# Performance work log

Hardware: AMD Instinct MI355X
Metric: run time of the kernel (lower is better)

Reference implementation:

```python
import jax, jax.numpy as jnp
import numpy as np

B, N, QD = 2, 2048, 1024
HEADS, DIM_HEAD = 16, 64
INNER = HEADS * DIM_HEAD  # 1024
SCALE = DIM_HEAD ** -0.5


def setup_inputs() -> dict:
    key = jax.random.key(0)
    ks = jax.random.split(key, 8)
    x = jax.random.normal(ks[0], (B, N, QD), dtype=jnp.float32)
    bias = jax.random.normal(ks[1], (B, N, N), dtype=jnp.float32)
    mask = jax.random.randint(ks[2], (B, N), 0, 2) > 0
    # parameters (nn.Linear stores weight [out, in]; we keep [in, out] and matmul x @ W)
    Wq = jax.random.normal(ks[3], (QD, INNER), dtype=jnp.float32) * (QD ** -0.5)
    Wkv = jax.random.normal(ks[4], (QD, 2 * INNER), dtype=jnp.float32) * (QD ** -0.5)
    Wo = jax.random.normal(ks[5], (INNER, QD), dtype=jnp.float32) * (INNER ** -0.5)
    bo = jax.random.normal(ks[6], (QD,), dtype=jnp.float32) * 0.01
    return {"x": x, "bias": bias, "mask": mask, "Wq": Wq, "Wkv": Wkv, "Wo": Wo, "bo": bo}


def reference(x, bias, mask, Wq, Wkv, Wo, bo):
    b, n, _ = x.shape
    q = x @ Wq                      # [b, n, inner]
    kv = x @ Wkv                    # [b, n, 2*inner] (context defaults to x)
    k, v = jnp.split(kv, 2, axis=-1)
    # split heads: [b, h, n, d]
    split = lambda t: t.reshape(b, n, HEADS, DIM_HEAD).transpose(0, 2, 1, 3)
    q, k, v = split(q), split(k), split(v)
    sim = jnp.einsum('bhid,bhjd->bhij', q, k) * SCALE   # [b, h, n, n]
    sim = sim + bias[:, None, :, :]                      # additive bias broadcast over heads
    max_neg = -jnp.finfo(sim.dtype).max
    sim = jnp.where(mask[:, None, None, :], sim, max_neg)  # per-key mask
    attn = jax.nn.softmax(sim, axis=-1)
    out = jnp.einsum('bhij,bhjd->bhid', attn, v)         # [b, h, n, d]
    out = out.transpose(0, 2, 1, 3).reshape(b, n, INNER)  # merge heads
    return out @ Wo + bo
```

## Files before the change

### kernel.cpp

```cpp
#include <hip/hip_runtime.h>
#include <hip/hip_bf16.h>
#include <stdint.h>

#define B_     2
#define N_     2048
#define QD_    1024
#define H_     16
#define DH_    64
#define INNER_ 1024
#define SCALE_ 0.125f
#define LOG2E_ 1.44269504f
#define QS_    (SCALE_ * LOG2E_)

typedef unsigned short u16;
typedef __attribute__((ext_vector_type(8))) short bf16x8;
typedef __attribute__((ext_vector_type(4))) float f32x4;
typedef __attribute__((ext_vector_type(4))) unsigned short u16x4;
typedef __attribute__((ext_vector_type(8))) unsigned short u16x8;

#define GLD16(gp, lp) __builtin_amdgcn_global_load_lds( \
    (const __attribute__((address_space(1))) unsigned int*)(gp), \
    (__attribute__((address_space(3))) unsigned int*)(lp), 16, 0, 0)

__device__ inline u16 f2bf(float f) {
    union { float f; uint32_t u; } c; c.f = f;
    uint32_t r = c.u + 0x7FFFu + ((c.u >> 16) & 1u);
    return (u16)(r >> 16);
}
__device__ inline float bf2f(u16 s) {
    union { uint32_t u; float f; } c; c.u = ((uint32_t)s) << 16;
    return c.f;
}
__device__ inline void split2(float v, u16 &h, u16 &l) {
    u16 hs = f2bf(v);
    h = hs;
    l = f2bf(v - bf2f(hs));
}
__device__ inline unsigned pk2(float a, float b) {
    float2 f; f.x = a; f.y = b;
    union { __hip_bfloat162 v; unsigned u; } c;
    c.v = __float22bfloat162_rn(f);
    return c.u;
}
__device__ inline float f4get(const float4& v, int r) {
    return r == 0 ? v.x : r == 1 ? v.y : r == 2 ? v.z : v.w;
}

__global__ __launch_bounds__(256) void prep_kernel(
    const float* __restrict__ x, u16* __restrict__ xh, u16* __restrict__ xl,
    const float* __restrict__ Wq, const float* __restrict__ Wkv, const float* __restrict__ Wo,
    u16* __restrict__ wTh, u16* __restrict__ wTl,
    u16* __restrict__ woTh, u16* __restrict__ woTl)
{
    __shared__ float t[32][33];
    const int blk = blockIdx.x, tid = threadIdx.x;
    if (blk < 4096) {
        int idx = blk * 256 + tid;
        float4 v = ((const float4*)x)[idx];
        u16x4 hv, lv; u16 h, l;
        split2(v.x, h, l); hv.x = h; lv.x = l;
        split2(v.y, h, l); hv.y = h; lv.y = l;
        split2(v.z, h, l); hv.z = h; lv.z = l;
        split2(v.w, h, l); hv.w = h; lv.w = l;
        ((u16x4*)xh)[idx] = hv;
        ((u16x4*)xl)[idx] = lv;
        return;
    }
    int local = blk - 4096;
    const float* src; u16 *dhi, *dlo; int C, bx, by;
    if (local < 1024)      { src = Wq;  dhi = wTh;                dlo = wTl;                C = 1024; by = local >> 5; bx = local & 31; }
    else if (local < 3072) { int l2 = local - 1024; src = Wkv; dhi = wTh + 1024 * 1024; dlo = wTl + 1024 * 1024; C = 2048; by = l2 >> 6; bx = l2 & 63; }
    else                   { int l2 = local - 3072; src = Wo;  dhi = woTh;               dlo = woTl;               C = 1024; by = l2 >> 5; bx = l2 & 31; }
    const int x0 = bx * 32, y0 = by * 32;
    const int tx = tid & 31, ty = tid >> 5;
    for (int yy = ty; yy < 32; yy += 8)
        t[yy][tx] = src[(size_t)(y0 + yy) * C + x0 + tx];
    __syncthreads();
    for (int i = ty; i < 32; i += 8) {
        float v = t[tx][i];
        u16 h, l; split2(v, h, l);
        size_t o = (size_t)(x0 + i) * 1024 + y0 + tx;
        dhi[o] = h; dlo[o] = l;
    }
}

__device__ inline void bias_read(int T, int bkoff, int bl16,
                                 const float* __restrict__ bias,
                                 const int* __restrict__ mask,
                                 float4 bR[4], int4& bM)
{
    int bb2 = T >> 10, rest = T & 1023;
    int k0b = (rest & 31) * 64, q0 = (rest >> 5) * 64;
    int kk = k0b + bkoff;
    bM = *(const int4*)&mask[bb2 * N_ + kk];
#pragma unroll
    for (int m = 0; m < 4; m++)
        bR[m] = *(const float4*)&bias[((size_t)bb2 * N_ + q0 + m * 16 + bl16) * N_ + kk];
}
__device__ inline void bias_store(int T, int bwvr, int blane, int bhf,
                                  const float4 bR[4], const int4& bM,
                                  u16* __restrict__ bsw)
{
    int bb2 = T >> 10, rest = T & 1023;
    int k0b = (rest & 31) * 64, q0 = (rest >> 5) * 64;
    int wv = ((k0b >> 5) & 3) + bwvr;
    const u16 NEG = f2bf(-1e30f);
    const int mok[4] = { bM.x, bM.y, bM.z, bM.w };
    u16x8 o0, o1;
#pragma unroll
    for (int i = 0; i < 8; i++) {
        int m = i >> 2, r = i & 3;
        o0[i] = mok[r] ? f2bf(f4get(bR[m], r) * LOG2E_) : NEG;
    }
#pragma unroll
    for (int i = 0; i < 8; i++) {
        int m = 2 + (i >> 2), r = i & 3;
        o1[i] = mok[r] ? f2bf(f4get(bR[m], r) * LOG2E_) : NEG;
    }
    size_t ob = ((((size_t)bb2 * 32 + (q0 >> 6)) * 16 + (k0b >> 7)) * 4 + wv) * 2048
                + (size_t)blane * 32 + bhf * 16;
    *(u16x8*)&bsw[ob]     = o0;
    *(u16x8*)&bsw[ob + 8] = o1;
}
__device__ inline void bias_block(int T, int tid,
                                  const float* __restrict__ bias,
                                  const int* __restrict__ mask,
                                  u16* __restrict__ bsw)
{
    const int bp = tid >> 1, bhf = tid & 1;
    const int blane = bp & 63, bquad = blane >> 4, bl16 = blane & 15;
    const int bwvr = bp >> 6;
    const int bkoff = bwvr * 32 + bquad * 8 + bhf * 4;
    float4 bR[4]; int4 bM;
    bias_read(T, bkoff, bl16, bias, mask, bR, bM);
    bias_store(T, bwvr, blane, bhf, bR, bM, bsw);
}

__global__ __launch_bounds__(256) void gemm_qkv_bias(
    int mode,
    const u16* __restrict__ Ah, const u16* __restrict__ Al,
    const u16* __restrict__ Bh,
    u16* __restrict__ qh,
    u16* __restrict__ kb, u16* __restrict__ vT,
    const float* __restrict__ bias, const int* __restrict__ mask,
    u16* __restrict__ bsw)
{
    __shared__ __align__(16) char smem[32768];
    const int tid = threadIdx.x;

    int gid = -1, bid = -1;
    if (mode == 1) {
        const int i = blockIdx.x;
        if (i < 1280) {
            int g = i % 5;
            if (g < 4) gid = (i / 5) * 4 + g;
            else       bid = i / 5;
        } else {
            bid = i - 1024;
        }
    } else if (mode == 0) gid = blockIdx.x;
    else bid = blockIdx.x;

    if (bid >= 0) {
        bias_block(bid, tid, bias, mask, bsw);
        return;
    }
    gid = (gid & 7) * 128 + (gid >> 3);

    const int wave = tid >> 6, lane = tid & 63;
    const int quad = lane >> 4, l16 = lane & 15;
    const int wm = wave >> 1, wn = wave & 1;
    const int row0 = tid >> 2, g4 = tid & 3;
    const int gc1 = (g4 ^ (row0 & 3)) * 8, gc2 = (g4 ^ ((row0 + 64) & 3)) * 8;
    const int ldsw = wave * 1024;

    if (gid < 512) {
        const int bm = (gid >> 4) * 128, bn = (8 + (gid & 15)) * 128;
        f32x4 acc[4][4];
#pragma unroll
        for (int i = 0; i < 4; i++)
#pragma unroll
            for (int j = 0; j < 4; j++) acc[i][j] = (f32x4){0.f, 0.f, 0.f, 0.f};

        const size_t a1 = (size_t)(bm + row0) * 1024 + gc1, a2 = (size_t)(bm + row0 + 64) * 1024 + gc2;
        const size_t b1 = (size_t)(bn + row0) * 1024 + gc1, b2 = (size_t)(bn + row0 + 64) * 1024 + gc2;

        auto issue = [&](char* base, int kn) {
            GLD16(Ah + a1 + kn, base + ldsw);
            GLD16(Ah + a2 + kn, base + 4096 + ldsw);
            GLD16(Bh + b1 + kn, base + 8192 + ldsw);
            GLD16(Bh + b2 + kn, base + 12288 + ldsw);
        };

        issue(smem, 0);
        int cur = 0;
        for (int k0 = 0; k0 < 1024; k0 += 32) {
            __syncthreads();
            char* cb_ = smem + cur * 16384;
            if (k0 + 32 < 1024) issue(smem + (cur ^ 1) * 16384, k0 + 32);
            const u16* cA = (const u16*)cb_;
            const u16* cB = (const u16*)(cb_ + 8192);
            bf16x8 fa[4], fb[4];
#pragma unroll
            for (int s = 0; s < 4; s++) {
                int ra = wm * 64 + s * 16 + l16;
                int rb = wn * 64 + s * 16 + l16;
                fa[s] = *(const bf16x8*)&cA[ra * 32 + (quad ^ (ra & 3)) * 8];
                fb[s] = *(const bf16x8*)&cB[rb * 32 + (quad ^ (rb & 3)) * 8];
            }
#pragma unroll
            for (int sm = 0; sm < 4; sm++)
#pragma unroll
                for (int sn = 0; sn < 4; sn++)
                    acc[sm][sn] = __builtin_amdgcn_mfma_f32_16x16x32_bf16(fa[sm], fb[sn], acc[sm][sn], 0, 0, 0);
            cur ^= 1;
        }
#pragma unroll
        for (int sm = 0; sm < 4; sm++) {
            int rowb = bm + wm * 64 + sm * 16 + quad * 4;
            int bb = rowb >> 11, i0 = rowb & 2047;
#pragma unroll
            for (int sn = 0; sn < 4; sn++) {
                int col = bn + wn * 64 + sn * 16 + l16;
                int region = col >> 10;
                int hh = (col >> 6) & 15;
                int d = col & 63;
                if (region == 1) {
#pragma unroll
                    for (int r = 0; r < 4; r++) {
                        size_t o = (((size_t)(bb * H_ + hh)) * N_ + i0 + r) * DH_ + d;
                        kb[o] = f2bf(acc[sm][sn][r]);
                    }
                } else {
                    u16x4 pv;
#pragma unroll
                    for (int r = 0; r < 4; r++) pv[r] = f2bf(acc[sm][sn][r]);
                    *(u16x4*)&vT[(((size_t)(bb * H_ + hh)) * DH_ + d) * N_ + i0] = pv;
                }
            }
        }
    } else {
        const int g2 = gid - 512;
        const int bm = (g2 >> 3) * 64, bn = (g2 & 7) * 128;
        f32x4 acc[2][4];
#pragma unroll
        for (int i = 0; i < 2; i++)
#pragma unroll
            for (int j = 0; j < 4; j++) acc[i][j] = (f32x4){0.f, 0.f, 0.f, 0.f};

        const size_t a1 = (size_t)(bm + row0) * 1024 + gc1;
        const size_t b1 = (size_t)(bn + row0) * 1024 + gc1, b2 = (size_t)(bn + row0 + 64) * 1024 + gc2;

        auto issue = [&](char* base, int kn) {
            GLD16(Ah + a1 + kn, base + ldsw);
            GLD16(Al + a1 + kn, base + 4096 + ldsw);
            GLD16(Bh + b1 + kn, base + 8192 + ldsw);
            GLD16(Bh + b2 + kn, base + 12288 + ldsw);
        };

        issue(smem, 0);
        int cur = 0;
        for (int k0 = 0; k0 < 1024; k0 += 32) {
            __syncthreads();
            char* cb_ = smem + cur * 16384;
            if (k0 + 32 < 1024) issue(smem + (cur ^ 1) * 16384, k0 + 32);
            const u16* cAh = (const u16*)cb_;
            const u16* cAl = (const u16*)(cb_ + 4096);
            const u16* cB  = (const u16*)(cb_ + 8192);
            bf16x8 fah[2], fal[2], fb[4];
#pragma unroll
            for (int s = 0; s < 2; s++) {
                int ra = wm * 32 + s * 16 + l16;
                int ca = (quad ^ (ra & 3)) * 8;
                fah[s] = *(const bf16x8*)&cAh[ra * 32 + ca];
                fal[s] = *(const bf16x8*)&cAl[ra * 32 + ca];
            }
#pragma unroll
            for (int s = 0; s < 4; s++) {
                int rb = wn * 64 + s * 16 + l16;
                fb[s] = *(const bf16x8*)&cB[rb * 32 + (quad ^ (rb & 3)) * 8];
            }
#pragma unroll
            for (int sm = 0; sm < 2; sm++)
#pragma unroll
                for (int sn = 0; sn < 4; sn++) {
                    acc[sm][sn] = __builtin_amdgcn_mfma_f32_16x16x32_bf16(fah[sm], fb[sn], acc[sm][sn], 0, 0, 0);
                    acc[sm][sn] = __builtin_amdgcn_mfma_f32_16x16x32_bf16(fal[sm], fb[sn], acc[sm][sn], 0, 0, 0);
                }
            cur ^= 1;
        }
#pragma unroll
        for (int sm = 0; sm < 2; sm++) {
            int rowb = bm + wm * 32 + sm * 16 + quad * 4;
            int bb = rowb >> 11, i0 = rowb & 2047;
#pragma unroll
            for (int sn = 0; sn < 4; sn++) {
                int col = bn + wn * 64 + sn * 16 + l16;
                int hh = col >> 6, d = col & 63;
#pragma unroll
                for (int r = 0; r < 4; r++) {
                    size_t o = (((size_t)(bb * H_ + hh)) * N_ + i0 + r) * DH_ + d;
                    qh[o] = f2bf(acc[sm][sn][r] * QS_);
                }
            }
        }
    }
}

__global__ __launch_bounds__(256) void gemm_out(
    const u16* __restrict__ Ab,
    const u16* __restrict__ Bh,
    const float* __restrict__ bo, float* __restrict__ out)
{
    __shared__ __align__(16) char smem[24576];
    const int tid = threadIdx.x;
    const int wave = tid >> 6, lane = tid & 63;
    const int quad = lane >> 4, l16 = lane & 15;
    const int wm = wave >> 1, wn = wave & 1;
    const int bm = blockIdx.y * 128, bn = blockIdx.x * 64;

    f32x4 acc[4][2];
#pragma unroll
    for (int i = 0; i < 4; i++)
#pragma unroll
        for (int j = 0; j < 2; j++) acc[i][j] = (f32x4){0.f, 0.f, 0.f, 0.f};

    const int row0 = tid >> 2, g4 = tid & 3;
    const int r1 = row0, r2 = row0 + 64;
    const int gc1 = (g4 ^ (r1 & 3)) * 8, gc2 = (g4 ^ (r2 & 3)) * 8;
    const size_t a1 = (size_t)(bm + r1) * 1024 + gc1, a2 = (size_t)(bm + r2) * 1024 + gc2;
    const size_t bgo = (size_t)(bn + r1) * 1024 + gc1;
    const int ldsw = wave * 1024;

    auto issue = [&](char* base, int kn) {
        GLD16(Ab + a1 + kn, base + ldsw);
        GLD16(Ab + a2 + kn, base + 4096 + ldsw);
        GLD16(Bh + bgo + kn, base + 8192 + ldsw);
    };

    issue(smem, 0);
    int cur = 0;
    for (int k0 = 0; k0 < 1024; k0 += 32) {
        __syncthreads();
        char* cb_ = smem + cur * 12288;
        if (k0 + 32 < 1024) issue(smem + (cur ^ 1) * 12288, k0 + 32);
        const u16* cA  = (const u16*)cb_;
        const u16* cBh = (const u16*)(cb_ + 8192);
        bf16x8 fa[4], fbh[2];
#pragma unroll
        for (int s = 0; s < 4; s++) {
            int ra = wm * 64 + s * 16 + l16;
            int ca = (quad ^ (ra & 3)) * 8;
            fa[s] = *(const bf16x8*)&cA[ra * 32 + ca];
        }
#pragma unroll
        for (int s = 0; s < 2; s++) {
            int rb = wn * 32 + s * 16 + l16;
            int cb = (quad ^ (rb & 3)) * 8;
            fbh[s] = *(const bf16x8*)&cBh[rb * 32 + cb];
        }
#pragma unroll
        for (int sm = 0; sm < 4; sm++)
#pragma unroll
            for (int sn = 0; sn < 2; sn++)
                acc[sm][sn] = __builtin_amdgcn_mfma_f32_16x16x32_bf16(fa[sm], fbh[sn], acc[sm][sn], 0, 0, 0);
        cur ^= 1;
    }
#pragma unroll
    for (int sm = 0; sm < 4; sm++) {
        int rowb = bm + wm * 64 + sm * 16 + quad * 4;
#pragma unroll
        for (int sn = 0; sn < 2; sn++) {
            int col = bn + wn * 32 + sn * 16 + l16;
            float bv = bo[col];
#pragma unroll
            for (int r = 0; r < 4; r++)
                out[(size_t)(rowb + r) * 1024 + col] = acc[sm][sn][r] + bv;
        }
    }
}

#define LDK 72
#define LDV 128

__global__ __launch_bounds__(256, 2) void attn_kernel(
    const u16* __restrict__ qh,
    const u16* __restrict__ kb, const u16* __restrict__ vT,
    const u16* __restrict__ bsw, u16* __restrict__ ob)
{
    __shared__ __align__(16) char smem[35328];
    u16* sK  = (u16*)smem;
    u16* sVt = (u16*)(smem + 18432);
    float* rO = (float*)smem;
    float* rL = (float*)(smem + 34816);

    const int bh = blockIdx.y, b = bh >> 4, h = bh & 15;
    const int qt = blockIdx.x, qbase = qt * 64;
    const int tid = threadIdx.x, wave = tid >> 6, lane = tid & 63;
    const int quad = lane >> 4, l16 = lane & 15;

    bf16x8 aq[4][2];
#pragma unroll
    for (int m = 0; m < 4; m++) {
        size_t qo = ((size_t)bh * N_ + qbase + m * 16 + l16) * DH_ + quad * 8;
        aq[m][0] = *(const bf16x8*)&qh[qo];
        aq[m][1] = *(const bf16x8*)&qh[qo + 32];
    }
    f32x4 Oacc[4][4], lacc[4];
#pragma unroll
    for (int m = 0; m < 4; m++) {
        lacc[m] = (f32x4){0.f, 0.f, 0.f, 0.f};
#pragma unroll
        for (int nd = 0; nd < 4; nd++) Oacc[m][nd] = (f32x4){0.f, 0.f, 0.f, 0.f};
    }
    bf16x8 ones;
#pragma unroll
    for (int i = 0; i < 8; i++) ones[i] = (short)0x3F80;

    const int rK = tid >> 3, cK = (tid & 7) * 8;
    const int sigK = ((rK & 4) << 2) + ((rK >> 3) << 2) + (rK & 3);
    const int rV = tid >> 4;
    const int vg = tid & 15;
    const int cV = vg * 8;
    const int vsw = (vg ^ (rV & 7)) * 8;
    const int vrg = ((wave * 4 + quad) ^ (l16 & 7)) * 8;
    const size_t kgbase = (size_t)bh * N_ * DH_;
    const size_t vgbase = (size_t)bh * DH_ * N_;
    const size_t bswb = (size_t)(b * 32 + qt) * 131072 + (size_t)wave * 2048
                        + (size_t)lane * 32;

    bf16x8 pK[4], pV[4];
    u16x8 cB[4], nB[4];
#pragma unroll
    for (int it = 0; it < 4; it++) {
        pK[it] = *(const bf16x8*)&kb[kgbase + (size_t)(rK + it * 32) * DH_ + cK];
        pV[it] = *(const bf16x8*)&vT[vgbase + (size_t)(rV + it * 16) * N_ + cV];
    }
#pragma unroll
    for (int c = 0; c < 4; c++) cB[c] = *(const u16x8*)&bsw[bswb + c * 8];

    for (int jt = 0; jt < 16; jt++) {
#pragma unroll
        for (int it = 0; it < 4; it++) {
            *(bf16x8*)&sK[(it * 32 + sigK) * LDK + cK] = pK[it];
            *(bf16x8*)&sVt[(rV + it * 16) * LDV + vsw] = pV[it];
        }
        __syncthreads();
        if (jt < 15) {
            int j0n = (jt + 1) * 128;
#pragma unroll
            for (int it = 0; it < 4; it++) {
                pK[it] = *(const bf16x8*)&kb[kgbase + (size_t)(j0n + rK + it * 32) * DH_ + cK];
                pV[it] = *(const bf16x8*)&vT[vgbase + (size_t)(rV + it * 16) * N_ + j0n + cV];
            }
            size_t bb = bswb + (size_t)(jt + 1) * 8192;
#pragma unroll
            for (int c = 0; c < 4; c++) nB[c] = *(const u16x8*)&bsw[bb + c * 8];
        }
        bf16x8 kf[2][2], vf[4];
#pragma unroll
        for (int n = 0; n < 2; n++)
#pragma unroll
            for (int s = 0; s < 2; s++)
                kf[n][s] = *(const bf16x8*)&sK[(wave * 32 + n * 16 + l16) * LDK + s * 32 + quad * 8];
#pragma unroll
        for (int nd = 0; nd < 4; nd++)
            vf[nd] = *(const bf16x8*)&sVt[(nd * 16 + l16) * LDV + vrg];

#pragma unroll
        for (int m = 0; m < 4; m++) {
            f32x4 S0, S1;
#pragma unroll
            for (int r = 0; r < 4; r++) {
                S0[r] = bf2f(cB[m >> 1][(m & 1) * 4 + r]);
                S1[r] = bf2f(cB[2 + (m >> 1)][(m & 1) * 4 + r]);
            }
#pragma unroll
            for (int s = 0; s < 2; s++) {
                S0 = __builtin_amdgcn_mfma_f32_16x16x32_bf16(kf[0][s], aq[m][s], S0, 0, 0, 0);
                S1 = __builtin_amdgcn_mfma_f32_16x16x32_bf16(kf[1][s], aq[m][s], S1, 0, 0, 0);
            }
            float p0[4], p1[4];
#pragma unroll
            for (int r = 0; r < 4; r++) {
                p0[r] = __builtin_amdgcn_exp2f(S0[r]);
                p1[r] = __builtin_amdgcn_exp2f(S1[r]);
            }
            union { bf16x8 v; unsigned w[4]; } pa;
            pa.w[0] = pk2(p0[0], p0[1]);
            pa.w[1] = pk2(p0[2], p0[3]);
            pa.w[2] = pk2(p1[0], p1[1]);
            pa.w[3] = pk2(p1[2], p1[3]);
            lacc[m] = __builtin_amdgcn_mfma_f32_16x16x32_bf16(pa.v, ones, lacc[m], 0, 0, 0);
#pragma unroll
            for (int nd = 0; nd < 4; nd++)
                Oacc[m][nd] = __builtin_amdgcn_mfma_f32_16x16x32_bf16(pa.v, vf[nd], Oacc[m][nd], 0, 0, 0);
        }
#pragma unroll
        for (int c = 0; c < 4; c++) cB[c] = nB[c];
        __syncthreads();
    }

    if (wave >= 2) {
        int slot = wave - 2;
#pragma unroll
        for (int m = 0; m < 4; m++) {
#pragma unroll
            for (int nd = 0; nd < 4; nd++)
#pragma unroll
                for (int r = 0; r < 4; r++)
                    rO[(slot * 64 + m * 16 + quad * 4 + r) * 68 + nd * 16 + l16] = Oacc[m][nd][r];
            if (l16 == 0)
#pragma unroll
                for (int r = 0; r < 4; r++)
                    rL[slot * 64 + m * 16 + quad * 4 + r] = lacc[m][r];
        }
    }
    __syncthreads();
    if (wave < 2) {
        int slot = wave;
#pragma unroll
        for (int m = 0; m < 4; m++) {
#pragma unroll
            for (int nd = 0; nd < 4; nd++)
#pragma unroll
                for (int r = 0; r < 4; r++) {
                    int idx = (slot * 64 + m * 16 + quad * 4 + r) * 68 + nd * 16 + l16;
                    rO[idx] += Oacc[m][nd][r];
                }
            if (l16 == 0)
#pragma unroll
                for (int r = 0; r < 4; r++)
                    rL[slot * 64 + m * 16 + quad * 4 + r] += lacc[m][r];
        }
    }
    __syncthreads();
    {
        const int q = tid >> 2, dg = (tid & 3) * 16;
        float l = rL[q] + rL[64 + q];
        float inv = 1.f / l;
        f32x4 s[4];
#pragma unroll
        for (int i4 = 0; i4 < 4; i4++) {
            s[i4] = *(const f32x4*)&rO[(size_t)q * 68 + dg + i4 * 4];
            f32x4 v = *(const f32x4*)&rO[(size_t)(64 + q) * 68 + dg + i4 * 4];
            s[i4] += v;
        }
        size_t obase = ((size_t)b * N_ + qbase + q) * INNER_ + h * 64 + dg;
#pragma unroll
        for (int i4 = 0; i4 < 4; i4++) {
            u16x4 o4;
#pragma unroll
            for (int r = 0; r < 4; r++) o4[r] = f2bf(s[i4][r] * inv);
            *(u16x4*)&ob[obase + i4 * 4] = o4;
        }
    }
}

extern "C" void kernel_launch(void* const* d_in, const int* in_sizes, int n_in,
                              void* d_out, int out_size, void* d_ws, size_t ws_size,
                              hipStream_t stream)
{
    const float* x    = (const float*)d_in[0];
    const float* bias = (const float*)d_in[1];
    const int*   mask = (const int*)d_in[2];
    const float* Wq   = (const float*)d_in[3];
    const float* Wkv  = (const float*)d_in[4];
    const float* Wo   = (const float*)d_in[5];
    const float* bo   = (const float*)d_in[6];
    float* out = (float*)d_out;

    char* w = (char*)d_ws;
    const size_t MB = 1024 * 1024;
    u16* q_h   = (u16*)(w);
    u16* k_b   = (u16*)(w + 16 * MB);
    u16* v_T   = (u16*)(w + 24 * MB);
    u16* xs_h  = (u16*)(w + 32 * MB);
    u16* xs_l  = (u16*)(w + 40 * MB);
    u16* wT_h  = (u16*)(w + 48 * MB);
    u16* wT_l  = (u16*)(w + 54 * MB);
    u16* woT_h = (u16*)(w + 60 * MB);
    u16* woT_l = (u16*)(w + 62 * MB);
    u16* o_b   = (u16*)(w + 64 * MB);

    const size_t bsw_bytes = (size_t)2 * N_ * N_ * sizeof(u16);
    const bool concurrent = ws_size >= 72 * MB + bsw_bytes;

    prep_kernel<<<8192, 256, 0, stream>>>(x, xs_h, xs_l, Wq, Wkv, Wo, wT_h, wT_l, woT_h, woT_l);

    if (concurrent) {
        u16* bsw = (u16*)(w + 72 * MB);
        gemm_qkv_bias<<<3072, 256, 0, stream>>>(1, xs_h, xs_l, wT_h,
                                                q_h, k_b, v_T, bias, mask, bsw);
        attn_kernel<<<dim3(32, 32), 256, 0, stream>>>(q_h, k_b, v_T, bsw, o_b);
    } else {
        u16* bsw = (u16*)(w + 32 * MB);
        gemm_qkv_bias<<<1024, 256, 0, stream>>>(0, xs_h, xs_l, wT_h,
                                                q_h, k_b, v_T, bias, mask, bsw);
        gemm_qkv_bias<<<2048, 256, 0, stream>>>(2, xs_h, xs_l, wT_h,
                                                q_h, k_b, v_T, bias, mask, bsw);
        attn_kernel<<<dim3(32, 32), 256, 0, stream>>>(q_h, k_b, v_T, bsw, o_b);
    }
    gemm_out<<<dim3(16, 32), 256, 0, stream>>>(o_b, woT_h, bo, out);
}
```

Measured before the change: 233.2 us.

## Split attention work across 8 waves by key group and query half

The attention kernel now launches 512 threads per block. Each wave owns one of four key sub-tiles and one of two query halves, so it holds half the Q fragments and accumulators it held before. The K/V staging loads and the bias reads are redistributed over the extra threads, and the epilogue writes 8-wide bf16 stores. The aim is more waves to hide latency and lower per-thread register pressure, at the cost of each wave re-reading the same K/V LDS fragments and more threads meeting at each barrier.

```diff
diff --git a/kernel.cpp b/kernel.cpp
--- a/kernel.cpp
+++ b/kernel.cpp
@@ -383,7 +383,7 @@
 #define LDK 72
 #define LDV 128
 
-__global__ __launch_bounds__(256, 2) void attn_kernel(
+__global__ __launch_bounds__(512, 2) void attn_kernel(
     const u16* __restrict__ qh,
     const u16* __restrict__ kb, const u16* __restrict__ vT,
     const u16* __restrict__ bsw, u16* __restrict__ ob)
@@ -398,87 +398,88 @@
     const int qt = blockIdx.x, qbase = qt * 64;
     const int tid = threadIdx.x, wave = tid >> 6, lane = tid & 63;
     const int quad = lane >> 4, l16 = lane & 15;
-
-    bf16x8 aq[4][2];
-#pragma unroll
-    for (int m = 0; m < 4; m++) {
-        size_t qo = ((size_t)bh * N_ + qbase + m * 16 + l16) * DH_ + quad * 8;
-        aq[m][0] = *(const bf16x8*)&qh[qo];
-        aq[m][1] = *(const bf16x8*)&qh[qo + 32];
-    }
-    f32x4 Oacc[4][4], lacc[4];
-#pragma unroll
-    for (int m = 0; m < 4; m++) {
-        lacc[m] = (f32x4){0.f, 0.f, 0.f, 0.f};
-#pragma unroll
-        for (int nd = 0; nd < 4; nd++) Oacc[m][nd] = (f32x4){0.f, 0.f, 0.f, 0.f};
+    const int kg = wave & 3, mg = wave >> 2;
+
+    bf16x8 aq[2][2];
+#pragma unroll
+    for (int mm = 0; mm < 2; mm++) {
+        size_t qo = ((size_t)bh * N_ + qbase + (mg * 2 + mm) * 16 + l16) * DH_ + quad * 8;
+        aq[mm][0] = *(const bf16x8*)&qh[qo];
+        aq[mm][1] = *(const bf16x8*)&qh[qo + 32];
+    }
+    f32x4 Oacc[2][4], lacc[2];
+#pragma unroll
+    for (int mm = 0; mm < 2; mm++) {
+        lacc[mm] = (f32x4){0.f, 0.f, 0.f, 0.f};
+#pragma unroll
+        for (int nd = 0; nd < 4; nd++) Oacc[mm][nd] = (f32x4){0.f, 0.f, 0.f, 0.f};
     }
     bf16x8 ones;
 #pragma unroll
     for (int i = 0; i < 8; i++) ones[i] = (short)0x3F80;
 
     const int rK = tid >> 3, cK = (tid & 7) * 8;
-    const int sigK = ((rK & 4) << 2) + ((rK >> 3) << 2) + (rK & 3);
+    const int sigK = (rK & 32) + ((rK & 4) << 2) + (((rK >> 3) & 3) << 2) + (rK & 3);
     const int rV = tid >> 4;
     const int vg = tid & 15;
     const int cV = vg * 8;
     const int vsw = (vg ^ (rV & 7)) * 8;
-    const int vrg = ((wave * 4 + quad) ^ (l16 & 7)) * 8;
+    const int vrg = ((kg * 4 + quad) ^ (l16 & 7)) * 8;
     const size_t kgbase = (size_t)bh * N_ * DH_;
     const size_t vgbase = (size_t)bh * DH_ * N_;
-    const size_t bswb = (size_t)(b * 32 + qt) * 131072 + (size_t)wave * 2048
-                        + (size_t)lane * 32;
-
-    bf16x8 pK[4], pV[4];
-    u16x8 cB[4], nB[4];
-#pragma unroll
-    for (int it = 0; it < 4; it++) {
-        pK[it] = *(const bf16x8*)&kb[kgbase + (size_t)(rK + it * 32) * DH_ + cK];
-        pV[it] = *(const bf16x8*)&vT[vgbase + (size_t)(rV + it * 16) * N_ + cV];
-    }
-#pragma unroll
-    for (int c = 0; c < 4; c++) cB[c] = *(const u16x8*)&bsw[bswb + c * 8];
+    const size_t bswb = (size_t)(b * 32 + qt) * 131072 + (size_t)kg * 2048
+                        + (size_t)lane * 32 + (size_t)mg * 8;
+
+    bf16x8 pK[2], pV[2];
+    u16x8 cB[2], nB[2];
+#pragma unroll
+    for (int it = 0; it < 2; it++) {
+        pK[it] = *(const bf16x8*)&kb[kgbase + (size_t)(rK + it * 64) * DH_ + cK];
+        pV[it] = *(const bf16x8*)&vT[vgbase + (size_t)(rV + it * 32) * N_ + cV];
+    }
+#pragma unroll
+    for (int c = 0; c < 2; c++) cB[c] = *(const u16x8*)&bsw[bswb + c * 16];
 
     for (int jt = 0; jt < 16; jt++) {
 #pragma unroll
-        for (int it = 0; it < 4; it++) {
-            *(bf16x8*)&sK[(it * 32 + sigK) * LDK + cK] = pK[it];
-            *(bf16x8*)&sVt[(rV + it * 16) * LDV + vsw] = pV[it];
+        for (int it = 0; it < 2; it++) {
+            *(bf16x8*)&sK[(it * 64 + sigK) * LDK + cK] = pK[it];
+            *(bf16x8*)&sVt[(rV + it * 32) * LDV + vsw] = pV[it];
         }
         __syncthreads();
         if (jt < 15) {
             int j0n = (jt + 1) * 128;
 #pragma unroll
-            for (int it = 0; it < 4; it++) {
-                pK[it] = *(const bf16x8*)&kb[kgbase + (size_t)(j0n + rK + it * 32) * DH_ + cK];
-                pV[it] = *(const bf16x8*)&vT[vgbase + (size_t)(rV + it * 16) * N_ + j0n + cV];
+            for (int it = 0; it < 2; it++) {
+                pK[it] = *(const bf16x8*)&kb[kgbase + (size_t)(j0n + rK + it * 64) * DH_ + cK];
+                pV[it] = *(const bf16x8*)&vT[vgbase + (size_t)(rV + it * 32) * N_ + j0n + cV];
             }
             size_t bb = bswb + (size_t)(jt + 1) * 8192;
 #pragma unroll
-            for (int c = 0; c < 4; c++) nB[c] = *(const u16x8*)&bsw[bb + c * 8];
+            for (int c = 0; c < 2; c++) nB[c] = *(const u16x8*)&bsw[bb + c * 16];
         }
         bf16x8 kf[2][2], vf[4];
 #pragma unroll
         for (int n = 0; n < 2; n++)
 #pragma unroll
             for (int s = 0; s < 2; s++)
-                kf[n][s] = *(const bf16x8*)&sK[(wave * 32 + n * 16 + l16) * LDK + s * 32 + quad * 8];
+                kf[n][s] = *(const bf16x8*)&sK[(kg * 32 + n * 16 + l16) * LDK + s * 32 + quad * 8];
 #pragma unroll
         for (int nd = 0; nd < 4; nd++)
             vf[nd] = *(const bf16x8*)&sVt[(nd * 16 + l16) * LDV + vrg];
 
 #pragma unroll
-        for (int m = 0; m < 4; m++) {
+        for (int mm = 0; mm < 2; mm++) {
             f32x4 S0, S1;
 #pragma unroll
             for (int r = 0; r < 4; r++) {
-                S0[r] = bf2f(cB[m >> 1][(m & 1) * 4 + r]);
-                S1[r] = bf2f(cB[2 + (m >> 1)][(m & 1) * 4 + r]);
+                S0[r] = bf2f(cB[0][mm * 4 + r]);
+                S1[r] = bf2f(cB[1][mm * 4 + r]);
             }
 #pragma unroll
             for (int s = 0; s < 2; s++) {
-                S0 = __builtin_amdgcn_mfma_f32_16x16x32_bf16(kf[0][s], aq[m][s], S0, 0, 0, 0);
-                S1 = __builtin_amdgcn_mfma_f32_16x16x32_bf16(kf[1][s], aq[m][s], S1, 0, 0, 0);
+                S0 = __builtin_amdgcn_mfma_f32_16x16x32_bf16(kf[0][s], aq[mm][s], S0, 0, 0, 0);
+                S1 = __builtin_amdgcn_mfma_f32_16x16x32_bf16(kf[1][s], aq[mm][s], S1, 0, 0, 0);
             }
             float p0[4], p1[4];
 #pragma unroll
@@ -491,69 +492,68 @@
             pa.w[1] = pk2(p0[2], p0[3]);
             pa.w[2] = pk2(p1[0], p1[1]);
             pa.w[3] = pk2(p1[2], p1[3]);
-            lacc[m] = __builtin_amdgcn_mfma_f32_16x16x32_bf16(pa.v, ones, lacc[m], 0, 0, 0);
+            lacc[mm] = __builtin_amdgcn_mfma_f32_16x16x32_bf16(pa.v, ones, lacc[mm], 0, 0, 0);
 #pragma unroll
             for (int nd = 0; nd < 4; nd++)
-                Oacc[m][nd] = __builtin_amdgcn_mfma_f32_16x16x32_bf16(pa.v, vf[nd], Oacc[m][nd], 0, 0, 0);
-        }
-#pragma unroll
-        for (int c = 0; c < 4; c++) cB[c] = nB[c];
+                Oacc[mm][nd] = __builtin_amdgcn_mfma_f32_16x16x32_bf16(pa.v, vf[nd], Oacc[mm][nd], 0, 0, 0);
+        }
+#pragma unroll
+        for (int c = 0; c < 2; c++) cB[c] = nB[c];
         __syncthreads();
     }
 
-    if (wave >= 2) {
-        int slot = wave - 2;
-#pragma unroll
-        for (int m = 0; m < 4; m++) {
+    if (kg >= 2) {
+        int slot = kg - 2;
+#pragma unroll
+        for (int mm = 0; mm < 2; mm++) {
+            int rbase = slot * 64 + mg * 32 + mm * 16 + quad * 4;
 #pragma unroll
             for (int nd = 0; nd < 4; nd++)
 #pragma unroll
                 for (int r = 0; r < 4; r++)
-                    rO[(slot * 64 + m * 16 + quad * 4 + r) * 68 + nd * 16 + l16] = Oacc[m][nd][r];
+                    rO[(rbase + r) * 68 + nd * 16 + l16] = Oacc[mm][nd][r];
             if (l16 == 0)
 #pragma unroll
                 for (int r = 0; r < 4; r++)
-                    rL[slot * 64 + m * 16 + quad * 4 + r] = lacc[m][r];
+                    rL[rbase + r] = lacc[mm][r];
         }
     }
     __syncthreads();
-    if (wave < 2) {
-        int slot = wave;
-#pragma unroll
-        for (int m = 0; m < 4; m++) {
+    if (kg < 2) {
+        int slot = kg;
+#pragma unroll
+        for (int mm = 0; mm < 2; mm++) {
+            int rbase = slot * 64 + mg * 32 + mm * 16 + quad * 4;
 #pragma unroll
             for (int nd = 0; nd < 4; nd++)
 #pragma unroll
                 for (int r = 0; r < 4; r++) {
-                    int idx = (slot * 64 + m * 16 + quad * 4 + r) * 68 + nd * 16 + l16;
-                    rO[idx] += Oacc[m][nd][r];
+                    int idx = (rbase + r) * 68 + nd * 16 + l16;
+                    rO[idx] += Oacc[mm][nd][r];
                 }
             if (l16 == 0)
 #pragma unroll
                 for (int r = 0; r < 4; r++)
-                    rL[slot * 64 + m * 16 + quad * 4 + r] += lacc[m][r];
+                    rL[rbase + r] += lacc[mm][r];
         }
     }
     __syncthreads();
     {
-        const int q = tid >> 2, dg = (tid & 3) * 16;
+        const int q = tid >> 3, dg = (tid & 7) * 8;
         float l = rL[q] + rL[64 + q];
         float inv = 1.f / l;
-        f32x4 s[4];
-#pragma unroll
-        for (int i4 = 0; i4 < 4; i4++) {
-            s[i4] = *(const f32x4*)&rO[(size_t)q * 68 + dg + i4 * 4];
-            f32x4 v = *(const f32x4*)&rO[(size_t)(64 + q) * 68 + dg + i4 * 4];
-            s[i4] += v;
-        }
+        f32x4 s0 = *(const f32x4*)&rO[(size_t)q * 68 + dg];
+        f32x4 s1 = *(const f32x4*)&rO[(size_t)q * 68 + dg + 4];
+        f32x4 t0 = *(const f32x4*)&rO[(size_t)(64 + q) * 68 + dg];
+        f32x4 t1 = *(const f32x4*)&rO[(size_t)(64 + q) * 68 + dg + 4];
+        s0 += t0; s1 += t1;
         size_t obase = ((size_t)b * N_ + qbase + q) * INNER_ + h * 64 + dg;
-#pragma unroll
-        for (int i4 = 0; i4 < 4; i4++) {
-            u16x4 o4;
-#pragma unroll
-            for (int r = 0; r < 4; r++) o4[r] = f2bf(s[i4][r] * inv);
-            *(u16x4*)&ob[obase + i4 * 4] = o4;
-        }
+        u16x8 o8;
+#pragma unroll
+        for (int r = 0; r < 4; r++) o8[r] = f2bf(s0[r] * inv);
+#pragma unroll
+        for (int r = 0; r < 4; r++) o8[4 + r] = f2bf(s1[r] * inv);
+        *(u16x8*)&ob[obase] = o8;
     }
 }
 
@@ -592,14 +592,14 @@
         u16* bsw = (u16*)(w + 72 * MB);
         gemm_qkv_bias<<<3072, 256, 0, stream>>>(1, xs_h, xs_l, wT_h,
                                                 q_h, k_b, v_T, bias, mask, bsw);
-        attn_kernel<<<dim3(32, 32), 256, 0, stream>>>(q_h, k_b, v_T, bsw, o_b);
+        attn_kernel<<<dim3(32, 32), 512, 0, stream>>>(q_h, k_b, v_T, bsw, o_b);
     } else {
         u16* bsw = (u16*)(w + 32 * MB);
         gemm_qkv_bias<<<1024, 256, 0, stream>>>(0, xs_h, xs_l, wT_h,
                                                 q_h, k_b, v_T, bias, mask, bsw);
         gemm_qkv_bias<<<2048, 256, 0, stream>>>(2, xs_h, xs_l, wT_h,
                                                 q_h, k_b, v_T, bias, mask, bsw);
-        attn_kernel<<<dim3(32, 32), 256, 0, stream>>>(q_h, k_b, v_T, bsw, o_b);
+        attn_kernel<<<dim3(32, 32), 512, 0, stream>>>(q_h, k_b, v_T, bsw, o_b);
     }
     gemm_out<<<dim3(16, 32), 256, 0, stream>>>(o_b, woT_h, bo, out);
 }
```

New measurement: 245.3 us. 5.2% more time.
